# Performance work log

Hardware: AMD Instinct MI355X
Metric: run time of the kernel (lower is better)

Reference implementation:

```python
import jax, jax.numpy as jnp
import numpy as np

sp = jax.nn.softplus


def hip_block(x, W1, b1, W2, b2):
    # HIPResidual: out = a(L1(x)); out = a(L2(out) + x)
    h = sp(x @ W1 + b1)
    return sp(h @ W2 + b2 + x)


def res_stack(x, Ws1, bs1, Ws2, bs2):
    for i in range(Ws1.shape[0]):  # fixed small n_res=3
        x = hip_block(x, Ws1[i], bs1[i], Ws2[i], bs2[i])
    return x


def setup_inputs() -> dict:
    key = jax.random.key(0)
    ks = jax.random.split(key, 24)
    B, A, F, R, P, NRES = 64, 256, 80, 20, 393216, 3
    N = B * A
    s = 0.05
    inp = {
        "species": jax.random.randint(ks[0], (B, A), 0, 5),
        "features": jax.random.normal(ks[1], (N, F), jnp.float32),
        "radial_aev": jax.random.uniform(ks[2], (P, R), jnp.float32),
        "atom_index12": jax.random.randint(ks[3], (2, P), 0, N),
        "WI": jax.random.normal(ks[4], (F, F), jnp.float32) * s,
        "bI": jnp.zeros((F,), jnp.float32),
        "Wg": jax.random.normal(ks[5], (R, F), jnp.float32) * s,
        "bg": jnp.zeros((F,), jnp.float32),
        "WJ": jax.random.normal(ks[6], (F, F), jnp.float32) * s,
        "bJ": jnp.zeros((F,), jnp.float32),
        "iW1": jax.random.normal(ks[7], (NRES, F, F), jnp.float32) * s,
        "ib1": jnp.zeros((NRES, F), jnp.float32),
        "iW2": jax.random.normal(ks[8], (NRES, F, F), jnp.float32) * s,
        "ib2": jnp.zeros((NRES, F), jnp.float32),
        "gate": jnp.ones((F,), jnp.float32),
        "Wint": jax.random.normal(ks[9], (F, F), jnp.float32) * s,
        "bint": jnp.zeros((F,), jnp.float32),
        "aW1": jax.random.normal(ks[10], (NRES, F, F), jnp.float32) * s,
        "ab1": jnp.zeros((NRES, F), jnp.float32),
        "aW2": jax.random.normal(ks[11], (NRES, F, F), jnp.float32) * s,
        "ab2": jnp.zeros((NRES, F), jnp.float32),
        "oW1": jax.random.normal(ks[12], (NRES, F, F), jnp.float32) * s,
        "ob1": jnp.zeros((NRES, F), jnp.float32),
        "oW2": jax.random.normal(ks[13], (NRES, F, F), jnp.float32) * s,
        "ob2": jnp.zeros((NRES, F), jnp.float32),
        "Wout": jax.random.normal(ks[14], (F, 1), jnp.float32) * s,
        "bout": jnp.zeros((1,), jnp.float32),
    }
    return inp


def reference(species, features, radial_aev, atom_index12,
              WI, bI, Wg, bg, WJ, bJ,
              iW1, ib1, iW2, ib2,
              gate, Wint, bint,
              aW1, ab1, aW2, ab2,
              oW1, ob1, oW2, ob2,
              Wout, bout):
    B, A = species.shape
    N, F = features.shape
    # dummy-atom mask (species == -1 rows are excluded in the original via
    # index_select/index_add; all per-atom ops are row-wise so masking is exact)
    mask = (species.reshape(-1) != -1).astype(features.dtype)[:, None]  # [N,1]

    # pair message: gather -> gated small MLP -> scatter-add
    f12 = features[atom_index12]                       # [2,P,F]
    aev_term = radial_aev @ Wg + bg                    # [P,F]
    fmsg = sp(sp(f12) @ WJ + bJ)                       # [2,P,F]
    pair_msg = aev_term[None] * fmsg                   # [2,P,F]

    proto = jnp.zeros_like(features).at[atom_index12.reshape(-1)].add(
        pair_msg.reshape(-1, F))
    proto = proto + (features @ WI + bI) * mask        # no-interaction term

    message = res_stack(proto, iW1, ib1, iW2, ib2)
    nd = features * gate[None, :] + sp(message) @ Wint + bint
    nd = res_stack(nd, aW1, ab1, aW2, ab2)
    energies = (sp(res_stack(nd, oW1, ob1, oW2, ob2)) @ Wout + bout)[:, 0]

    out_energies = (energies * mask[:, 0]).reshape(B, A)
    out_features = nd * mask
    return out_energies, out_features
```

## Files before the change

### kernel.cpp

```cpp
#include <hip/hip_runtime.h>
#include <hip/hip_bf16.h>

#define FDIM 80
#define RDIM 20
#define NSLOT 6
#define LDP  104
#define WROW 96
#define AROWS 32

#define FIX_SCALE 512.0f
#define FIX_INV   0.001953125f

typedef float  f32x4  __attribute__((ext_vector_type(4)));
typedef short  bf16x8 __attribute__((ext_vector_type(8)));

__device__ __forceinline__ float sp_f(float x){
  float e = __expf(-fabsf(x));
  return fmaxf(x, 0.f) + __logf(1.f + e);
}
__device__ __forceinline__ __hip_bfloat16 tob(float x){ return __float2bfloat16(x); }

struct WPtrs { const float* p[21]; };

__global__ __launch_bounds__(256) void prep_weights(WPtrs wp, __hip_bfloat16* __restrict__ wt){
  const float* W = wp.p[blockIdx.x];
  __hip_bfloat16* dst = wt + (size_t)blockIdx.x * FDIM * WROW;
  for (int i = threadIdx.x; i < FDIM * WROW; i += 256){
    int j = i / WROW, k = i - j * WROW;
    dst[i] = __float2bfloat16(k < FDIM ? W[k * FDIM + j] : 0.f);
  }
}

__global__ __launch_bounds__(256) void scatter_p16(const float* __restrict__ aev,
    const int* __restrict__ idx12, unsigned long long* __restrict__ R6u, int P)
{
  int g = blockIdx.x * 256 + threadIdx.x;
  if (g >= P * NSLOT) return;
  int p = g / NSLOT, s = g - p * NSLOT;
  unsigned long long v;
  if (s < 5){
    float4 a = ((const float4*)(aev + (size_t)p * RDIM))[s];
    unsigned long long f0 = (unsigned long long)__float2uint_rn(a.x * FIX_SCALE);
    unsigned long long f1 = (unsigned long long)__float2uint_rn(a.y * FIX_SCALE);
    unsigned long long f2 = (unsigned long long)__float2uint_rn(a.z * FIX_SCALE);
    unsigned long long f3 = (unsigned long long)__float2uint_rn(a.w * FIX_SCALE);
    v = f0 | (f1 << 16) | (f2 << 32) | (f3 << 48);
  } else {
    v = 512ULL;
  }
  int i1 = idx12[p], i2 = idx12[P + p];
  atomicAdd(&R6u[(size_t)i1 * NSLOT + s], v);
  atomicAdd(&R6u[(size_t)i2 * NSLOT + s], v);
}

struct WF { bf16x8 b0, b1, b2; float bias; };

__device__ __forceinline__ WF loadWF(const __hip_bfloat16* __restrict__ wb,
                                     int slot, const float* __restrict__ bias, int row){
  WF w;
  const __hip_bfloat16* p = wb + (size_t)slot * (FDIM * WROW);
  w.b0 = *(const bf16x8*)(const void*)(p);
  w.b1 = *(const bf16x8*)(const void*)(p + 32);
  w.b2 = *(const bf16x8*)(const void*)(p + 64);
  w.bias = bias[row];
  return w;
}

__device__ __forceinline__ void mfmaL(f32x4 acc[2],
    const __hip_bfloat16 (*in)[LDP], int j0, int kb, const WF& w)
{
  #pragma unroll
  for (int s = 0; s < 2; s++){
    const __hip_bfloat16* ap = &in[16*s + j0][kb];
    bf16x8 a0 = *(const bf16x8*)(const void*)(ap);
    bf16x8 a1 = *(const bf16x8*)(const void*)(ap + 32);
    bf16x8 a2 = *(const bf16x8*)(const void*)(ap + 64);
    acc[s] = (f32x4){w.bias, w.bias, w.bias, w.bias};
    acc[s] = __builtin_amdgcn_mfma_f32_16x16x32_bf16(a0, w.b0, acc[s], 0, 0, 0);
    acc[s] = __builtin_amdgcn_mfma_f32_16x16x32_bf16(a1, w.b1, acc[s], 0, 0, 0);
    acc[s] = __builtin_amdgcn_mfma_f32_16x16x32_bf16(a2, w.b2, acc[s], 0, 0, 0);
  }
}

__device__ __forceinline__ void resblk(f32x4 cur[2],
    __hip_bfloat16 (*bA)[LDP], __hip_bfloat16 (*bB)[LDP],
    int j0, int kb, int g, int col,
    WF& w1, WF& w2,
    const __hip_bfloat16* __restrict__ wb, int row,
    int pf1, const float* __restrict__ pf1b,
    int pf2, const float* __restrict__ pf2b)
{
  f32x4 acc[2];
  mfmaL(acc, bA, j0, kb, w1);
  w1 = loadWF(wb, pf1, pf1b, row);
  #pragma unroll
  for (int s = 0; s < 2; s++){
    int r0 = 16*s + g*4;
    #pragma unroll
    for (int i = 0; i < 4; i++) bB[r0 + i][col] = tob(sp_f(acc[s][i]));
  }
  __syncthreads();
  mfmaL(acc, bB, j0, kb, w2);
  w2 = loadWF(wb, pf2, pf2b, row);
  #pragma unroll
  for (int s = 0; s < 2; s++){
    int r0 = 16*s + g*4;
    #pragma unroll
    for (int i = 0; i < 4; i++){
      cur[s][i] = sp_f(acc[s][i] + cur[s][i]);
      bA[r0 + i][col] = tob(cur[s][i]);
    }
  }
  __syncthreads();
}

__global__ __launch_bounds__(320, 4) void atom_mfma(
    const int*   __restrict__ species,
    const float* __restrict__ features,
    const unsigned long long* __restrict__ R6u,
    const __hip_bfloat16* __restrict__ wt,
    const float* __restrict__ Wg, const float* __restrict__ bg,
    const float* __restrict__ bJ, const float* __restrict__ bI,
    const float* __restrict__ ib1, const float* __restrict__ ib2,
    const float* __restrict__ gate, const float* __restrict__ bint,
    const float* __restrict__ ab1, const float* __restrict__ ab2,
    const float* __restrict__ ob1, const float* __restrict__ ob2,
    const float* __restrict__ Wout, const float* __restrict__ bout,
    float* __restrict__ out_e, float* __restrict__ out_f)
{
  __shared__ __align__(16) __hip_bfloat16 bufA[AROWS][LDP];
  __shared__ __align__(16) __hip_bfloat16 bufB[AROWS][LDP];
  __shared__ __align__(16) __hip_bfloat16 xfb[AROWS][LDP];
  __shared__ float Rl[AROWS][4 * NSLOT];
  __shared__ float mskl[AROWS];
  __shared__ float evp[5][AROWS];

  const int t    = threadIdx.x;
  const int lane = t & 63;
  const int nt   = t >> 6;
  const int base = blockIdx.x * AROWS;

  const int j0  = lane & 15;
  const int g   = lane >> 4;
  const int kb  = g * 8;
  const int col = 16*nt + j0;
  const int row = col;
  const __hip_bfloat16* wb = wt + (size_t)row * WROW + kb;

  float wgc[RDIM];
  #pragma unroll
  for (int r = 0; r < RDIM; r++) wgc[r] = Wg[r * FDIM + col];
  const float bgv = bg[col];

  for (int i = t; i < AROWS * FDIM; i += 320){
    int rr = i / FDIM, cc = i - rr * FDIM;
    float v = features[(size_t)(base + rr) * FDIM + cc];
    xfb [rr][cc] = tob(v);
    bufA[rr][cc] = tob(sp_f(v));
  }
  for (int i = t; i < 3 * AROWS * 16; i += 320){
    int b = i / (AROWS * 16), rem = i % (AROWS * 16);
    int rr = rem >> 4, cc = FDIM + (rem & 15);
    if      (b == 0) bufA[rr][cc] = tob(0.f);
    else if (b == 1) bufB[rr][cc] = tob(0.f);
    else             xfb [rr][cc] = tob(0.f);
  }
  if (t < AROWS * NSLOT){
    int u = t / NSLOT, s5 = t - u * NSLOT;
    unsigned long long v = R6u[(size_t)(base + u) * NSLOT + s5];
    #pragma unroll
    for (int f = 0; f < 4; f++)
      Rl[u][4*s5 + f] = (float)((unsigned int)(v >> (16*f)) & 0xffffu) * FIX_INV;
  }
  if (t < AROWS) mskl[t] = (species[base + t] != -1) ? 1.f : 0.f;
  __syncthreads();

  f32x4 Sreg[2];
  #pragma unroll
  for (int s = 0; s < 2; s++){
    #pragma unroll
    for (int i = 0; i < 4; i++){
      int rr = 16*s + g*4 + i;
      float a = Rl[rr][RDIM] * bgv;
      #pragma unroll
      for (int r = 0; r < RDIM; r++) a += Rl[rr][r] * wgc[r];
      Sreg[s][i] = a;
    }
  }

  f32x4 cur[2];

  {
    WF wA = loadWF(wb, 0, bJ, row);
    WF wB = loadWF(wb, 1, bI, row);
    f32x4 aJ[2], aI[2];
    mfmaL(aJ, bufA, j0, kb, wA);  wA = loadWF(wb, 3, ib1, row);
    mfmaL(aI, xfb , j0, kb, wB);  wB = loadWF(wb, 4, ib2, row);
    __syncthreads();
    #pragma unroll
    for (int s = 0; s < 2; s++){
      int r0 = 16*s + g*4;
      #pragma unroll
      for (int i = 0; i < 4; i++){
        cur[s][i] = sp_f(aJ[s][i]) * Sreg[s][i] + aI[s][i] * mskl[r0 + i];
        bufA[r0 + i][col] = tob(cur[s][i]);
      }
    }
    __syncthreads();

    resblk(cur, bufA, bufB, j0, kb, g, col, wA, wB, wb, row,
           5, ib1 + FDIM,     6, ib2 + FDIM);
    resblk(cur, bufA, bufB, j0, kb, g, col, wA, wB, wb, row,
           7, ib1 + 2*FDIM,   8, ib2 + 2*FDIM);
    resblk(cur, bufA, bufB, j0, kb, g, col, wA, wB, wb, row,
           2, bint,           9, ab1);

    #pragma unroll
    for (int s = 0; s < 2; s++){
      int r0 = 16*s + g*4;
      #pragma unroll
      for (int i = 0; i < 4; i++) bufB[r0 + i][col] = tob(sp_f(cur[s][i]));
    }
    __syncthreads();
    {
      f32x4 acc[2];
      mfmaL(acc, bufB, j0, kb, wA);
      wA = loadWF(wb, 10, ab2, row);
      float gj = gate[col];
      #pragma unroll
      for (int s = 0; s < 2; s++){
        int r0 = 16*s + g*4;
        #pragma unroll
        for (int i = 0; i < 4; i++){
          float xv = __bfloat162float(xfb[r0 + i][col]);
          cur[s][i] = xv * gj + acc[s][i];
          bufA[r0 + i][col] = tob(cur[s][i]);
        }
      }
    }
    __syncthreads();

    resblk(cur, bufA, bufB, j0, kb, g, col, wB, wA, wb, row,
           11, ab1 + FDIM,    12, ab2 + FDIM);
    resblk(cur, bufA, bufB, j0, kb, g, col, wB, wA, wb, row,
           13, ab1 + 2*FDIM,  14, ab2 + 2*FDIM);
    resblk(cur, bufA, bufB, j0, kb, g, col, wB, wA, wb, row,
           15, ob1,           16, ob2);

    #pragma unroll
    for (int s = 0; s < 2; s++){
      int r0 = 16*s + g*4;
      #pragma unroll
      for (int i = 0; i < 4; i++)
        out_f[(size_t)(base + r0 + i) * FDIM + col] = cur[s][i] * mskl[r0 + i];
    }

    resblk(cur, bufA, bufB, j0, kb, g, col, wB, wA, wb, row,
           17, ob1 + FDIM,    18, ob2 + FDIM);
    resblk(cur, bufA, bufB, j0, kb, g, col, wB, wA, wb, row,
           19, ob1 + 2*FDIM,  20, ob2 + 2*FDIM);
    resblk(cur, bufA, bufB, j0, kb, g, col, wB, wA, wb, row,
           0, bJ,             0, bJ);
  }

  {
    float wv = Wout[col];
    float ev[2][4];
    #pragma unroll
    for (int s = 0; s < 2; s++)
      #pragma unroll
      for (int i = 0; i < 4; i++) ev[s][i] = sp_f(cur[s][i]) * wv;
    #pragma unroll
    for (int off = 1; off < 16; off <<= 1){
      #pragma unroll
      for (int s = 0; s < 2; s++)
        #pragma unroll
        for (int i = 0; i < 4; i++) ev[s][i] += __shfl_xor(ev[s][i], off);
    }
    if (j0 == 0){
      #pragma unroll
      for (int s = 0; s < 2; s++)
        #pragma unroll
        for (int i = 0; i < 4; i++) evp[nt][16*s + g*4 + i] = ev[s][i];
    }
  }
  __syncthreads();
  if (t < AROWS)
    out_e[base + t] = (evp[0][t] + evp[1][t] + evp[2][t] + evp[3][t] + evp[4][t]
                       + bout[0]) * mskl[t];
}

extern "C" void kernel_launch(void* const* d_in, const int* in_sizes, int n_in,
                              void* d_out, int out_size, void* d_ws, size_t ws_size,
                              hipStream_t stream) {
  const int*   species  = (const int*)  d_in[0];
  const float* features = (const float*)d_in[1];
  const float* aev      = (const float*)d_in[2];
  const int*   idx12    = (const int*)  d_in[3];
  const float* WI   = (const float*)d_in[4];  const float* bI   = (const float*)d_in[5];
  const float* Wg   = (const float*)d_in[6];  const float* bg   = (const float*)d_in[7];
  const float* WJ   = (const float*)d_in[8];  const float* bJ   = (const float*)d_in[9];
  const float* iW1  = (const float*)d_in[10]; const float* ib1  = (const float*)d_in[11];
  const float* iW2  = (const float*)d_in[12]; const float* ib2  = (const float*)d_in[13];
  const float* gate = (const float*)d_in[14];
  const float* Wint = (const float*)d_in[15]; const float* bint = (const float*)d_in[16];
  const float* aW1  = (const float*)d_in[17]; const float* ab1  = (const float*)d_in[18];
  const float* aW2  = (const float*)d_in[19]; const float* ab2  = (const float*)d_in[20];
  const float* oW1  = (const float*)d_in[21]; const float* ob1  = (const float*)d_in[22];
  const float* oW2  = (const float*)d_in[23]; const float* ob2  = (const float*)d_in[24];
  const float* Wout = (const float*)d_in[25]; const float* bout = (const float*)d_in[26];

  const int N = in_sizes[1] / FDIM;
  const int P = in_sizes[2] / RDIM;

  unsigned long long* R6u = (unsigned long long*)d_ws;
  __hip_bfloat16* wt = (__hip_bfloat16*)(R6u + (size_t)N * NSLOT);

  float* out_e = (float*)d_out;
  float* out_f = out_e + N;

  hipMemsetAsync(R6u, 0, (size_t)N * NSLOT * sizeof(unsigned long long), stream);

  WPtrs wp;
  wp.p[0] = WJ; wp.p[1] = WI; wp.p[2] = Wint;
  for (int ir = 0; ir < 3; ir++){
    wp.p[3  + 2*ir] = iW1 + ir*FDIM*FDIM; wp.p[4  + 2*ir] = iW2 + ir*FDIM*FDIM;
    wp.p[9  + 2*ir] = aW1 + ir*FDIM*FDIM; wp.p[10 + 2*ir] = aW2 + ir*FDIM*FDIM;
    wp.p[15 + 2*ir] = oW1 + ir*FDIM*FDIM; wp.p[16 + 2*ir] = oW2 + ir*FDIM*FDIM;
  }
  prep_weights<<<21, 256, 0, stream>>>(wp, wt);

  scatter_p16<<<((size_t)P * NSLOT + 255) / 256, 256, 0, stream>>>(aev, idx12, R6u, P);

  atom_mfma<<<(N + AROWS - 1) / AROWS, 320, 0, stream>>>(species, features, R6u, wt,
      Wg, bg, bJ, bI, ib1, ib2, gate, bint, ab1, ab2, ob1, ob2, Wout, bout,
      out_e, out_f);
}
```

Before: 107.0 us.

## Pack pair-count into 13-bit fixed-point slots and halve atom tile rows

```diff
diff --git a/kernel.cpp b/kernel.cpp
--- a/kernel.cpp
+++ b/kernel.cpp
@@ -3,13 +3,13 @@
 
 #define FDIM 80
 #define RDIM 20
-#define NSLOT 6
+#define RSLOT 5
 #define LDP  104
 #define WROW 96
-#define AROWS 32
-
-#define FIX_SCALE 512.0f
-#define FIX_INV   0.001953125f
+#define AROWS 16
+
+#define FIX_SCALE 64.0f
+#define FIX_INV   0.015625f
 
 typedef float  f32x4  __attribute__((ext_vector_type(4)));
 typedef short  bf16x8 __attribute__((ext_vector_type(8)));
@@ -31,26 +31,22 @@
   }
 }
 
-__global__ __launch_bounds__(256) void scatter_p16(const float* __restrict__ aev,
-    const int* __restrict__ idx12, unsigned long long* __restrict__ R6u, int P)
+__global__ __launch_bounds__(256) void scatter_p13(const float* __restrict__ aev,
+    const int* __restrict__ idx12, unsigned long long* __restrict__ R5u, int P)
 {
   int g = blockIdx.x * 256 + threadIdx.x;
-  if (g >= P * NSLOT) return;
-  int p = g / NSLOT, s = g - p * NSLOT;
-  unsigned long long v;
-  if (s < 5){
-    float4 a = ((const float4*)(aev + (size_t)p * RDIM))[s];
-    unsigned long long f0 = (unsigned long long)__float2uint_rn(a.x * FIX_SCALE);
-    unsigned long long f1 = (unsigned long long)__float2uint_rn(a.y * FIX_SCALE);
-    unsigned long long f2 = (unsigned long long)__float2uint_rn(a.z * FIX_SCALE);
-    unsigned long long f3 = (unsigned long long)__float2uint_rn(a.w * FIX_SCALE);
-    v = f0 | (f1 << 16) | (f2 << 32) | (f3 << 48);
-  } else {
-    v = 512ULL;
-  }
+  if (g >= P * RSLOT) return;
+  int p = g / RSLOT, s = g - p * RSLOT;
+  float4 a = ((const float4*)(aev + (size_t)p * RDIM))[s];
+  unsigned long long f0 = (unsigned long long)__float2uint_rn(a.x * FIX_SCALE);
+  unsigned long long f1 = (unsigned long long)__float2uint_rn(a.y * FIX_SCALE);
+  unsigned long long f2 = (unsigned long long)__float2uint_rn(a.z * FIX_SCALE);
+  unsigned long long f3 = (unsigned long long)__float2uint_rn(a.w * FIX_SCALE);
+  unsigned long long v = f0 | (f1 << 13) | (f2 << 26) | (f3 << 39);
+  if (s == 0) v |= (1ULL << 52);
   int i1 = idx12[p], i2 = idx12[P + p];
-  atomicAdd(&R6u[(size_t)i1 * NSLOT + s], v);
-  atomicAdd(&R6u[(size_t)i2 * NSLOT + s], v);
+  atomicAdd(&R5u[(size_t)i1 * RSLOT + s], v);
+  atomicAdd(&R5u[(size_t)i2 * RSLOT + s], v);
 }
 
 struct WF { bf16x8 b0, b1, b2; float bias; };
@@ -66,23 +62,21 @@
   return w;
 }
 
-__device__ __forceinline__ void mfmaL(f32x4 acc[2],
+__device__ __forceinline__ f32x4 mfmaL(
     const __hip_bfloat16 (*in)[LDP], int j0, int kb, const WF& w)
 {
-  #pragma unroll
-  for (int s = 0; s < 2; s++){
-    const __hip_bfloat16* ap = &in[16*s + j0][kb];
-    bf16x8 a0 = *(const bf16x8*)(const void*)(ap);
-    bf16x8 a1 = *(const bf16x8*)(const void*)(ap + 32);
-    bf16x8 a2 = *(const bf16x8*)(const void*)(ap + 64);
-    acc[s] = (f32x4){w.bias, w.bias, w.bias, w.bias};
-    acc[s] = __builtin_amdgcn_mfma_f32_16x16x32_bf16(a0, w.b0, acc[s], 0, 0, 0);
-    acc[s] = __builtin_amdgcn_mfma_f32_16x16x32_bf16(a1, w.b1, acc[s], 0, 0, 0);
-    acc[s] = __builtin_amdgcn_mfma_f32_16x16x32_bf16(a2, w.b2, acc[s], 0, 0, 0);
-  }
-}
-
-__device__ __forceinline__ void resblk(f32x4 cur[2],
+  const __hip_bfloat16* ap = &in[j0][kb];
+  bf16x8 a0 = *(const bf16x8*)(const void*)(ap);
+  bf16x8 a1 = *(const bf16x8*)(const void*)(ap + 32);
+  bf16x8 a2 = *(const bf16x8*)(const void*)(ap + 64);
+  f32x4 acc = (f32x4){w.bias, w.bias, w.bias, w.bias};
+  acc = __builtin_amdgcn_mfma_f32_16x16x32_bf16(a0, w.b0, acc, 0, 0, 0);
+  acc = __builtin_amdgcn_mfma_f32_16x16x32_bf16(a1, w.b1, acc, 0, 0, 0);
+  acc = __builtin_amdgcn_mfma_f32_16x16x32_bf16(a2, w.b2, acc, 0, 0, 0);
+  return acc;
+}
+
+__device__ __forceinline__ void resblk(f32x4& cur,
     __hip_bfloat16 (*bA)[LDP], __hip_bfloat16 (*bB)[LDP],
     int j0, int kb, int g, int col,
     WF& w1, WF& w2,
@@ -90,26 +84,17 @@
     int pf1, const float* __restrict__ pf1b,
     int pf2, const float* __restrict__ pf2b)
 {
-  f32x4 acc[2];
-  mfmaL(acc, bA, j0, kb, w1);
+  f32x4 acc = mfmaL(bA, j0, kb, w1);
   w1 = loadWF(wb, pf1, pf1b, row);
   #pragma unroll
-  for (int s = 0; s < 2; s++){
-    int r0 = 16*s + g*4;
-    #pragma unroll
-    for (int i = 0; i < 4; i++) bB[r0 + i][col] = tob(sp_f(acc[s][i]));
-  }
-  __syncthreads();
-  mfmaL(acc, bB, j0, kb, w2);
+  for (int i = 0; i < 4; i++) bB[g*4 + i][col] = tob(sp_f(acc[i]));
+  __syncthreads();
+  acc = mfmaL(bB, j0, kb, w2);
   w2 = loadWF(wb, pf2, pf2b, row);
   #pragma unroll
-  for (int s = 0; s < 2; s++){
-    int r0 = 16*s + g*4;
-    #pragma unroll
-    for (int i = 0; i < 4; i++){
-      cur[s][i] = sp_f(acc[s][i] + cur[s][i]);
-      bA[r0 + i][col] = tob(cur[s][i]);
-    }
+  for (int i = 0; i < 4; i++){
+    cur[i] = sp_f(acc[i] + cur[i]);
+    bA[g*4 + i][col] = tob(cur[i]);
   }
   __syncthreads();
 }
@@ -117,7 +102,7 @@
 __global__ __launch_bounds__(320, 4) void atom_mfma(
     const int*   __restrict__ species,
     const float* __restrict__ features,
-    const unsigned long long* __restrict__ R6u,
+    const unsigned long long* __restrict__ R5u,
     const __hip_bfloat16* __restrict__ wt,
     const float* __restrict__ Wg, const float* __restrict__ bg,
     const float* __restrict__ bJ, const float* __restrict__ bI,
@@ -131,7 +116,7 @@
   __shared__ __align__(16) __hip_bfloat16 bufA[AROWS][LDP];
   __shared__ __align__(16) __hip_bfloat16 bufB[AROWS][LDP];
   __shared__ __align__(16) __hip_bfloat16 xfb[AROWS][LDP];
-  __shared__ float Rl[AROWS][4 * NSLOT];
+  __shared__ float Rl[AROWS][22];
   __shared__ float mskl[AROWS];
   __shared__ float evp[5][AROWS];
 
@@ -147,10 +132,10 @@
   const int row = col;
   const __hip_bfloat16* wb = wt + (size_t)row * WROW + kb;
 
-  float wgc[RDIM];
+  float wgc[RDIM + 1];
   #pragma unroll
   for (int r = 0; r < RDIM; r++) wgc[r] = Wg[r * FDIM + col];
-  const float bgv = bg[col];
+  wgc[RDIM] = bg[col];
 
   for (int i = t; i < AROWS * FDIM; i += 320){
     int rr = i / FDIM, cc = i - rr * FDIM;
@@ -165,46 +150,39 @@
     else if (b == 1) bufB[rr][cc] = tob(0.f);
     else             xfb [rr][cc] = tob(0.f);
   }
-  if (t < AROWS * NSLOT){
-    int u = t / NSLOT, s5 = t - u * NSLOT;
-    unsigned long long v = R6u[(size_t)(base + u) * NSLOT + s5];
+  if (t < AROWS * RSLOT){
+    int u = t / RSLOT, s5 = t - u * RSLOT;
+    unsigned long long v = R5u[(size_t)(base + u) * RSLOT + s5];
     #pragma unroll
     for (int f = 0; f < 4; f++)
-      Rl[u][4*s5 + f] = (float)((unsigned int)(v >> (16*f)) & 0xffffu) * FIX_INV;
+      Rl[u][4*s5 + f] = (float)((unsigned int)(v >> (13*f)) & 0x1fffu) * FIX_INV;
+    if (s5 == 0) Rl[u][RDIM] = (float)((unsigned int)(v >> 52) & 0xfffu);
   }
   if (t < AROWS) mskl[t] = (species[base + t] != -1) ? 1.f : 0.f;
   __syncthreads();
 
-  f32x4 Sreg[2];
-  #pragma unroll
-  for (int s = 0; s < 2; s++){
-    #pragma unroll
-    for (int i = 0; i < 4; i++){
-      int rr = 16*s + g*4 + i;
-      float a = Rl[rr][RDIM] * bgv;
-      #pragma unroll
-      for (int r = 0; r < RDIM; r++) a += Rl[rr][r] * wgc[r];
-      Sreg[s][i] = a;
-    }
-  }
-
-  f32x4 cur[2];
+  f32x4 Sreg;
+  #pragma unroll
+  for (int i = 0; i < 4; i++){
+    int rr = g*4 + i;
+    float a = 0.f;
+    #pragma unroll
+    for (int r = 0; r <= RDIM; r++) a += Rl[rr][r] * wgc[r];
+    Sreg[i] = a;
+  }
+
+  f32x4 cur;
 
   {
     WF wA = loadWF(wb, 0, bJ, row);
     WF wB = loadWF(wb, 1, bI, row);
-    f32x4 aJ[2], aI[2];
-    mfmaL(aJ, bufA, j0, kb, wA);  wA = loadWF(wb, 3, ib1, row);
-    mfmaL(aI, xfb , j0, kb, wB);  wB = loadWF(wb, 4, ib2, row);
-    __syncthreads();
-    #pragma unroll
-    for (int s = 0; s < 2; s++){
-      int r0 = 16*s + g*4;
-      #pragma unroll
-      for (int i = 0; i < 4; i++){
-        cur[s][i] = sp_f(aJ[s][i]) * Sreg[s][i] + aI[s][i] * mskl[r0 + i];
-        bufA[r0 + i][col] = tob(cur[s][i]);
-      }
+    f32x4 aJ = mfmaL(bufA, j0, kb, wA);  wA = loadWF(wb, 3, ib1, row);
+    f32x4 aI = mfmaL(xfb , j0, kb, wB);  wB = loadWF(wb, 4, ib2, row);
+    __syncthreads();
+    #pragma unroll
+    for (int i = 0; i < 4; i++){
+      cur[i] = sp_f(aJ[i]) * Sreg[i] + aI[i] * mskl[g*4 + i];
+      bufA[g*4 + i][col] = tob(cur[i]);
     }
     __syncthreads();
 
@@ -216,26 +194,17 @@
            2, bint,           9, ab1);
 
     #pragma unroll
-    for (int s = 0; s < 2; s++){
-      int r0 = 16*s + g*4;
-      #pragma unroll
-      for (int i = 0; i < 4; i++) bufB[r0 + i][col] = tob(sp_f(cur[s][i]));
-    }
+    for (int i = 0; i < 4; i++) bufB[g*4 + i][col] = tob(sp_f(cur[i]));
     __syncthreads();
     {
-      f32x4 acc[2];
-      mfmaL(acc, bufB, j0, kb, wA);
+      f32x4 acc = mfmaL(bufB, j0, kb, wA);
       wA = loadWF(wb, 10, ab2, row);
       float gj = gate[col];
       #pragma unroll
-      for (int s = 0; s < 2; s++){
-        int r0 = 16*s + g*4;
-        #pragma unroll
-        for (int i = 0; i < 4; i++){
-          float xv = __bfloat162float(xfb[r0 + i][col]);
-          cur[s][i] = xv * gj + acc[s][i];
-          bufA[r0 + i][col] = tob(cur[s][i]);
-        }
+      for (int i = 0; i < 4; i++){
+        float xv = __bfloat162float(xfb[g*4 + i][col]);
+        cur[i] = xv * gj + acc[i];
+        bufA[g*4 + i][col] = tob(cur[i]);
       }
     }
     __syncthreads();
@@ -248,12 +217,8 @@
            15, ob1,           16, ob2);
 
     #pragma unroll
-    for (int s = 0; s < 2; s++){
-      int r0 = 16*s + g*4;
-      #pragma unroll
-      for (int i = 0; i < 4; i++)
-        out_f[(size_t)(base + r0 + i) * FDIM + col] = cur[s][i] * mskl[r0 + i];
-    }
+    for (int i = 0; i < 4; i++)
+      out_f[(size_t)(base + g*4 + i) * FDIM + col] = cur[i] * mskl[g*4 + i];
 
     resblk(cur, bufA, bufB, j0, kb, g, col, wB, wA, wb, row,
            17, ob1 + FDIM,    18, ob2 + FDIM);
@@ -265,23 +230,17 @@
 
   {
     float wv = Wout[col];
-    float ev[2][4];
-    #pragma unroll
-    for (int s = 0; s < 2; s++)
-      #pragma unroll
-      for (int i = 0; i < 4; i++) ev[s][i] = sp_f(cur[s][i]) * wv;
+    float ev[4];
+    #pragma unroll
+    for (int i = 0; i < 4; i++) ev[i] = sp_f(cur[i]) * wv;
     #pragma unroll
     for (int off = 1; off < 16; off <<= 1){
       #pragma unroll
-      for (int s = 0; s < 2; s++)
-        #pragma unroll
-        for (int i = 0; i < 4; i++) ev[s][i] += __shfl_xor(ev[s][i], off);
+      for (int i = 0; i < 4; i++) ev[i] += __shfl_xor(ev[i], off);
     }
     if (j0 == 0){
       #pragma unroll
-      for (int s = 0; s < 2; s++)
-        #pragma unroll
-        for (int i = 0; i < 4; i++) evp[nt][16*s + g*4 + i] = ev[s][i];
+      for (int i = 0; i < 4; i++) evp[nt][g*4 + i] = ev[i];
     }
   }
   __syncthreads();
@@ -313,13 +272,13 @@
   const int N = in_sizes[1] / FDIM;
   const int P = in_sizes[2] / RDIM;
 
-  unsigned long long* R6u = (unsigned long long*)d_ws;
-  __hip_bfloat16* wt = (__hip_bfloat16*)(R6u + (size_t)N * NSLOT);
+  unsigned long long* R5u = (unsigned long long*)d_ws;
+  __hip_bfloat16* wt = (__hip_bfloat16*)(R5u + (size_t)N * RSLOT);
 
   float* out_e = (float*)d_out;
   float* out_f = out_e + N;
 
-  hipMemsetAsync(R6u, 0, (size_t)N * NSLOT * sizeof(unsigned long long), stream);
+  hipMemsetAsync(R5u, 0, (size_t)N * RSLOT * sizeof(unsigned long long), stream);
 
   WPtrs wp;
   wp.p[0] = WJ; wp.p[1] = WI; wp.p[2] = Wint;
@@ -330,9 +289,9 @@
   }
   prep_weights<<<21, 256, 0, stream>>>(wp, wt);
 
-  scatter_p16<<<((size_t)P * NSLOT + 255) / 256, 256, 0, stream>>>(aev, idx12, R6u, P);
-
-  atom_mfma<<<(N + AROWS - 1) / AROWS, 320, 0, stream>>>(species, features, R6u, wt,
+  scatter_p13<<<((size_t)P * RSLOT + 255) / 256, 256, 0, stream>>>(aev, idx12, R5u, P);
+
+  atom_mfma<<<(N + AROWS - 1) / AROWS, 320, 0, stream>>>(species, features, R5u, wt,
       Wg, bg, bJ, bI, ib1, ib2, gate, bint, ab1, ab2, ob1, ob2, Wout, bout,
       out_e, out_f);
 }
```

Measured after the change: 108.4 us. Within noise of the previous version (+1.3%).

## Replace global atomic pair scatter with two-pass bucketed binning and LDS accumulation

Applied to the files above, without the earlier changes.

```diff
diff --git a/kernel.cpp b/kernel.cpp
--- a/kernel.cpp
+++ b/kernel.cpp
@@ -3,13 +3,18 @@
 
 #define FDIM 80
 #define RDIM 20
-#define NSLOT 6
 #define LDP  104
 #define WROW 96
 #define AROWS 32
 
-#define FIX_SCALE 512.0f
-#define FIX_INV   0.001953125f
+#define NBUCK 512
+#define BCAP  2048
+#define CHUNK 4096
+#define RECW  12
+
+#define RSLOT 5
+#define FIX_SCALE 64.0f
+#define FIX_INV   0.015625f
 
 typedef float  f32x4  __attribute__((ext_vector_type(4)));
 typedef short  bf16x8 __attribute__((ext_vector_type(8)));
@@ -19,6 +24,14 @@
   return fmaxf(x, 0.f) + __logf(1.f + e);
 }
 __device__ __forceinline__ __hip_bfloat16 tob(float x){ return __float2bfloat16(x); }
+
+__device__ __forceinline__ unsigned bf16r(float f){
+  unsigned u = __float_as_uint(f);
+  return (u + 0x7fffu + ((u >> 16) & 1u)) >> 16;
+}
+__device__ __forceinline__ unsigned pk2(float x, float y){
+  return (bf16r(y) << 16) | bf16r(x);
+}
 
 struct WPtrs { const float* p[21]; };
 
@@ -31,26 +44,142 @@
   }
 }
 
-__global__ __launch_bounds__(256) void scatter_p16(const float* __restrict__ aev,
-    const int* __restrict__ idx12, unsigned long long* __restrict__ R6u, int P)
+__global__ __launch_bounds__(256) void binA(
+    const float* __restrict__ aev, const int* __restrict__ idx12,
+    int* __restrict__ gcursor, unsigned int* __restrict__ rec, int P)
+{
+  __shared__ int a_arr[CHUNK];
+  __shared__ unsigned int grp[CHUNK];
+  __shared__ unsigned short grpb[CHUNK];
+  __shared__ int cnt[NBUCK], cnt2[NBUCK], boff[NBUCK], gbase[NBUCK];
+  __shared__ int scanp[256];
+
+  const int t  = threadIdx.x;
+  const int c0 = blockIdx.x * CHUNK;
+
+  for (int b = t; b < NBUCK; b += 256){ cnt[b] = 0; cnt2[b] = 0; }
+  __syncthreads();
+  #pragma unroll
+  for (int k = 0; k < CHUNK / 256; k++){
+    int i = k * 256 + t;
+    int a = idx12[c0 + i];
+    a_arr[i] = a;
+    atomicAdd(&cnt[a >> 5], 1);
+  }
+  __syncthreads();
+  int cv0 = cnt[2*t], cv1 = cnt[2*t + 1];
+  scanp[t] = cv0 + cv1;
+  __syncthreads();
+  for (int off = 1; off < 256; off <<= 1){
+    int v = (t >= off) ? scanp[t - off] : 0;
+    __syncthreads();
+    scanp[t] += v;
+    __syncthreads();
+  }
+  int ex = (t == 0) ? 0 : scanp[t - 1];
+  boff[2*t] = ex; boff[2*t + 1] = ex + cv0;
+  for (int b = t; b < NBUCK; b += 256)
+    gbase[b] = atomicAdd(&gcursor[b], cnt[b]);
+  __syncthreads();
+  #pragma unroll
+  for (int k = 0; k < CHUNK / 256; k++){
+    int i = k * 256 + t;
+    int a = a_arr[i];
+    int b = a >> 5;
+    int e = c0 + i;
+    unsigned int p = (e < P) ? (unsigned)e : (unsigned)(e - P);
+    int slot = boff[b] + atomicAdd(&cnt2[b], 1);
+    grp[slot]  = (p << 5) | (unsigned)(a & 31);
+    grpb[slot] = (unsigned short)b;
+  }
+  __syncthreads();
+  #pragma unroll
+  for (int k = 0; k < CHUNK / 256; k++){
+    int slot = k * 256 + t;
+    unsigned int gv = grp[slot];
+    int b = grpb[slot];
+    unsigned int p = gv >> 5;
+    unsigned int local = gv & 31u;
+    int off = gbase[b] + (slot - boff[b]);
+    if (off >= BCAP) continue;
+    const float4* ar = (const float4*)(aev + (size_t)p * RDIM);
+    float4 a0 = ar[0], a1 = ar[1], a2 = ar[2], a3 = ar[3], a4 = ar[4];
+    uint4 w0, w1, w2;
+    w0.x = local;
+    w0.y = pk2(a0.x, a0.y); w0.z = pk2(a0.z, a0.w); w0.w = pk2(a1.x, a1.y);
+    w1.x = pk2(a1.z, a1.w); w1.y = pk2(a2.x, a2.y); w1.z = pk2(a2.z, a2.w); w1.w = pk2(a3.x, a3.y);
+    w2.x = pk2(a3.z, a3.w); w2.y = pk2(a4.x, a4.y); w2.z = pk2(a4.z, a4.w); w2.w = 0;
+    uint4* dst = (uint4*)(rec + ((size_t)b * BCAP + off) * RECW);
+    dst[0] = w0; dst[1] = w1; dst[2] = w2;
+  }
+}
+
+__global__ __launch_bounds__(256) void accumB(
+    const unsigned int* __restrict__ rec, const int* __restrict__ gcursor,
+    float* __restrict__ Rf)
+{
+  __shared__ float Racc[32][21];
+  const int t = threadIdx.x;
+  const int b = blockIdx.x;
+
+  for (int i = t; i < 32 * 21; i += 256) ((float*)Racc)[i] = 0.f;
+  __syncthreads();
+
+  const int cntb = min(gcursor[b], BCAP);
+  const unsigned int* rb = rec + (size_t)b * BCAP * RECW;
+  const int rloc = t >> 5;
+  const int c    = t & 31;
+
+  for (int r0 = 0; r0 < cntb; r0 += 8){
+    int r = r0 + rloc;
+    if (r < cntb){
+      const unsigned int* rp = rb + (size_t)r * RECW;
+      int local = (int)rp[0];
+      if (c < 20){
+        unsigned w = rp[1 + (c >> 1)];
+        unsigned h = (c & 1) ? (w >> 16) : (w & 0xffffu);
+        atomicAdd(&Racc[local][c], __uint_as_float(h << 16));
+      } else if (c == 20){
+        atomicAdd(&Racc[local][20], 1.f);
+      }
+    }
+  }
+  __syncthreads();
+  for (int i = t; i < 32 * 21; i += 256)
+    Rf[(size_t)b * (32 * 21) + i] = ((float*)Racc)[i];
+}
+
+__global__ __launch_bounds__(256) void scatter_p13(const float* __restrict__ aev,
+    const int* __restrict__ idx12, unsigned long long* __restrict__ R5u, int P)
 {
   int g = blockIdx.x * 256 + threadIdx.x;
-  if (g >= P * NSLOT) return;
-  int p = g / NSLOT, s = g - p * NSLOT;
-  unsigned long long v;
-  if (s < 5){
-    float4 a = ((const float4*)(aev + (size_t)p * RDIM))[s];
-    unsigned long long f0 = (unsigned long long)__float2uint_rn(a.x * FIX_SCALE);
-    unsigned long long f1 = (unsigned long long)__float2uint_rn(a.y * FIX_SCALE);
-    unsigned long long f2 = (unsigned long long)__float2uint_rn(a.z * FIX_SCALE);
-    unsigned long long f3 = (unsigned long long)__float2uint_rn(a.w * FIX_SCALE);
-    v = f0 | (f1 << 16) | (f2 << 32) | (f3 << 48);
-  } else {
-    v = 512ULL;
-  }
+  if (g >= P * RSLOT) return;
+  int p = g / RSLOT, s = g - p * RSLOT;
+  float4 a = ((const float4*)(aev + (size_t)p * RDIM))[s];
+  unsigned long long f0 = (unsigned long long)__float2uint_rn(a.x * FIX_SCALE);
+  unsigned long long f1 = (unsigned long long)__float2uint_rn(a.y * FIX_SCALE);
+  unsigned long long f2 = (unsigned long long)__float2uint_rn(a.z * FIX_SCALE);
+  unsigned long long f3 = (unsigned long long)__float2uint_rn(a.w * FIX_SCALE);
+  unsigned long long v = f0 | (f1 << 13) | (f2 << 26) | (f3 << 39);
+  if (s == 0) v |= (1ULL << 52);
   int i1 = idx12[p], i2 = idx12[P + p];
-  atomicAdd(&R6u[(size_t)i1 * NSLOT + s], v);
-  atomicAdd(&R6u[(size_t)i2 * NSLOT + s], v);
+  atomicAdd(&R5u[(size_t)i1 * RSLOT + s], v);
+  atomicAdd(&R5u[(size_t)i2 * RSLOT + s], v);
+}
+
+__global__ __launch_bounds__(256) void conv_p13(
+    const unsigned long long* __restrict__ R5u, float* __restrict__ Rf, int N)
+{
+  int n = blockIdx.x * 256 + threadIdx.x;
+  if (n >= N) return;
+  #pragma unroll
+  for (int s = 0; s < RSLOT; s++){
+    unsigned long long v = R5u[(size_t)n * RSLOT + s];
+    #pragma unroll
+    for (int f = 0; f < 4; f++)
+      Rf[(size_t)n * 21 + 4*s + f] = (float)((unsigned)(v >> (13*f)) & 0x1fffu) * FIX_INV;
+    if (s == 0) Rf[(size_t)n * 21 + RDIM] = (float)((unsigned)(v >> 52) & 0xfffu);
+  }
 }
 
 struct WF { bf16x8 b0, b1, b2; float bias; };
@@ -117,7 +246,7 @@
 __global__ __launch_bounds__(320, 4) void atom_mfma(
     const int*   __restrict__ species,
     const float* __restrict__ features,
-    const unsigned long long* __restrict__ R6u,
+    const float* __restrict__ Rf,
     const __hip_bfloat16* __restrict__ wt,
     const float* __restrict__ Wg, const float* __restrict__ bg,
     const float* __restrict__ bJ, const float* __restrict__ bI,
@@ -131,7 +260,7 @@
   __shared__ __align__(16) __hip_bfloat16 bufA[AROWS][LDP];
   __shared__ __align__(16) __hip_bfloat16 bufB[AROWS][LDP];
   __shared__ __align__(16) __hip_bfloat16 xfb[AROWS][LDP];
-  __shared__ float Rl[AROWS][4 * NSLOT];
+  __shared__ float Rl[AROWS][22];
   __shared__ float mskl[AROWS];
   __shared__ float evp[5][AROWS];
 
@@ -147,10 +276,10 @@
   const int row = col;
   const __hip_bfloat16* wb = wt + (size_t)row * WROW + kb;
 
-  float wgc[RDIM];
+  float wgc[RDIM + 1];
   #pragma unroll
   for (int r = 0; r < RDIM; r++) wgc[r] = Wg[r * FDIM + col];
-  const float bgv = bg[col];
+  wgc[RDIM] = bg[col];
 
   for (int i = t; i < AROWS * FDIM; i += 320){
     int rr = i / FDIM, cc = i - rr * FDIM;
@@ -165,12 +294,9 @@
     else if (b == 1) bufB[rr][cc] = tob(0.f);
     else             xfb [rr][cc] = tob(0.f);
   }
-  if (t < AROWS * NSLOT){
-    int u = t / NSLOT, s5 = t - u * NSLOT;
-    unsigned long long v = R6u[(size_t)(base + u) * NSLOT + s5];
-    #pragma unroll
-    for (int f = 0; f < 4; f++)
-      Rl[u][4*s5 + f] = (float)((unsigned int)(v >> (16*f)) & 0xffffu) * FIX_INV;
+  for (int i = t; i < AROWS * 21; i += 320){
+    int u = i / 21, r = i - u * 21;
+    Rl[u][r] = Rf[(size_t)base * 21 + i];
   }
   if (t < AROWS) mskl[t] = (species[base + t] != -1) ? 1.f : 0.f;
   __syncthreads();
@@ -181,9 +307,9 @@
     #pragma unroll
     for (int i = 0; i < 4; i++){
       int rr = 16*s + g*4 + i;
-      float a = Rl[rr][RDIM] * bgv;
-      #pragma unroll
-      for (int r = 0; r < RDIM; r++) a += Rl[rr][r] * wgc[r];
+      float a = 0.f;
+      #pragma unroll
+      for (int r = 0; r <= RDIM; r++) a += Rl[rr][r] * wgc[r];
       Sreg[s][i] = a;
     }
   }
@@ -313,13 +439,13 @@
   const int N = in_sizes[1] / FDIM;
   const int P = in_sizes[2] / RDIM;
 
-  unsigned long long* R6u = (unsigned long long*)d_ws;
-  __hip_bfloat16* wt = (__hip_bfloat16*)(R6u + (size_t)N * NSLOT);
-
   float* out_e = (float*)d_out;
   float* out_f = out_e + N;
 
-  hipMemsetAsync(R6u, 0, (size_t)N * NSLOT * sizeof(unsigned long long), stream);
+  const size_t REC_BYTES = (size_t)NBUCK * BCAP * (RECW * 4);
+  const size_t WT_BYTES  = (size_t)21 * FDIM * WROW * sizeof(__hip_bfloat16);
+  const size_t RF_BYTES  = (size_t)N * 21 * sizeof(float);
+  const size_t need = REC_BYTES + RF_BYTES + WT_BYTES + NBUCK * sizeof(int);
 
   WPtrs wp;
   wp.p[0] = WJ; wp.p[1] = WI; wp.p[2] = Wint;
@@ -328,11 +454,31 @@
     wp.p[9  + 2*ir] = aW1 + ir*FDIM*FDIM; wp.p[10 + 2*ir] = aW2 + ir*FDIM*FDIM;
     wp.p[15 + 2*ir] = oW1 + ir*FDIM*FDIM; wp.p[16 + 2*ir] = oW2 + ir*FDIM*FDIM;
   }
-  prep_weights<<<21, 256, 0, stream>>>(wp, wt);
-
-  scatter_p16<<<((size_t)P * NSLOT + 255) / 256, 256, 0, stream>>>(aev, idx12, R6u, P);
-
-  atom_mfma<<<(N + AROWS - 1) / AROWS, 320, 0, stream>>>(species, features, R6u, wt,
-      Wg, bg, bJ, bI, ib1, ib2, gate, bint, ab1, ab2, ob1, ob2, Wout, bout,
-      out_e, out_f);
-}
+
+  if (ws_size >= need){
+    unsigned int* rec = (unsigned int*)d_ws;
+    float* Rf = (float*)((char*)d_ws + REC_BYTES);
+    __hip_bfloat16* wt = (__hip_bfloat16*)((char*)Rf + RF_BYTES);
+    int* gcursor = (int*)((char*)wt + WT_BYTES);
+
+    hipMemsetAsync(gcursor, 0, NBUCK * sizeof(int), stream);
+    prep_weights<<<21, 256, 0, stream>>>(wp, wt);
+    binA<<<(2 * P) / CHUNK, 256, 0, stream>>>(aev, idx12, gcursor, rec, P);
+    accumB<<<NBUCK, 256, 0, stream>>>(rec, gcursor, Rf);
+    atom_mfma<<<(N + AROWS - 1) / AROWS, 320, 0, stream>>>(species, features, Rf, wt,
+        Wg, bg, bJ, bI, ib1, ib2, gate, bint, ab1, ab2, ob1, ob2, Wout, bout,
+        out_e, out_f);
+  } else {
+    unsigned long long* R5u = (unsigned long long*)d_ws;
+    float* Rf = (float*)(R5u + (size_t)N * RSLOT);
+    __hip_bfloat16* wt = (__hip_bfloat16*)((char*)Rf + RF_BYTES);
+
+    hipMemsetAsync(R5u, 0, (size_t)N * RSLOT * sizeof(unsigned long long), stream);
+    prep_weights<<<21, 256, 0, stream>>>(wp, wt);
+    scatter_p13<<<((size_t)P * RSLOT + 255) / 256, 256, 0, stream>>>(aev, idx12, R5u, P);
+    conv_p13<<<(N + 255) / 256, 256, 0, stream>>>(R5u, Rf, N);
+    atom_mfma<<<(N + AROWS - 1) / AROWS, 320, 0, stream>>>(species, features, Rf, wt,
+        Wg, bg, bJ, bI, ib1, ib2, gate, bint, ab1, ab2, ob1, ob2, Wout, bout,
+        out_e, out_f);
+  }
+}
```

Result: slower. 178.3 us (+66.6%).
